# Performance work log

Hardware: AMD Instinct MI355X
Metric: run time of the kernel (lower is better)

The kernel has to match this reference:

```python
import jax, jax.numpy as jnp
import numpy as np

B, N, K = 2, 16384, 8
NH, HD, CH, KV_IN = 4, 32, 128, 128
EPS = 1e-5

def layer_norm(x, g, b):
    mu = x.mean(-1, keepdims=True)
    var = ((x - mu) ** 2).mean(-1, keepdims=True)
    return (x - mu) / jnp.sqrt(var + EPS) * g + b

def setup_inputs() -> dict:
    key = jax.random.key(0)
    ks = jax.random.split(key, 8)
    s = 0.02
    return {
        "query_in": jax.random.normal(ks[0], (B, N, CH), jnp.float32),
        "kv_in": jax.random.normal(ks[1], (B, N, K, KV_IN), jnp.float32),
        "w_kv": jax.random.normal(ks[2], (KV_IN, 2 * NH * HD), jnp.float32) * s,
        "w_q": jax.random.normal(ks[3], (CH, NH * HD), jnp.float32) * s,
        "w_mh": jax.random.normal(ks[4], (NH * HD, CH), jnp.float32) * s,
        "b_mh": jnp.zeros((CH,), jnp.float32),
        "w1": jax.random.normal(ks[5], (CH, CH), jnp.float32) * s,
        "b1": jnp.zeros((CH,), jnp.float32),
        "w2": jax.random.normal(ks[6], (CH, CH), jnp.float32) * s,
        "b2": jnp.zeros((CH,), jnp.float32),
        "ln1_g": jnp.ones((CH,), jnp.float32),
        "ln1_b": jnp.zeros((CH,), jnp.float32),
        "ln2_g": jnp.ones((CH,), jnp.float32),
        "ln2_b": jnp.zeros((CH,), jnp.float32),
    }

def reference(query_in, kv_in, w_kv, w_q, w_mh, b_mh, w1, b1, w2, b2,
              ln1_g, ln1_b, ln2_g, ln2_b):
    # q projection: [B,N,CH] -> [B,N,NH,HD]
    q = (query_in @ w_q).reshape(B, N, NH, HD)
    # kv projection: [B,N,K,KV_IN] -> [B,N,K,2,NH,HD]; chunk(2) on last dim
    kv = (kv_in @ w_kv).reshape(B, N, K, 2, NH, HD)
    k, v = kv[..., 0, :, :], kv[..., 1, :, :]  # each [B,N,K,NH,HD]
    # per-token local attention over its own K keys
    sim = jnp.einsum('bnhd,bnkhd->bnhk', q, k) / np.sqrt(HD).astype(np.float32)
    attn = jax.nn.softmax(sim, axis=-1)
    out = jnp.einsum('bnhk,bnkhd->bnhd', attn, v).reshape(B, N, NH * HD)
    out = out @ w_mh + b_mh
    res = layer_norm(out, ln1_g, ln1_b) + query_in
    # GELU MLP (torch nn.GELU default = exact erf form)
    mlp = jax.nn.gelu(res @ w1 + b1, approximate=False) @ w2 + b2
    return layer_norm(mlp + res, ln2_g, ln2_b)
```

## Files before the change

### kernel.cpp

```cpp
#include <hip/hip_runtime.h>
#include <hip/hip_fp16.h>

typedef _Float16 f16x8 __attribute__((ext_vector_type(8)));
typedef float f32x4 __attribute__((ext_vector_type(4)));
typedef unsigned int uint32;

#define LDW 136
#define TB  16

#define WAITLGKM() do { __builtin_amdgcn_s_waitcnt(0xC07F); __builtin_amdgcn_sched_barrier(0); } while(0)

#define BAR() do {                                          \
  asm volatile("s_waitcnt lgkmcnt(0)" ::: "memory");        \
  __builtin_amdgcn_sched_barrier(0);                        \
  __builtin_amdgcn_s_barrier();                             \
  __builtin_amdgcn_sched_barrier(0);                        \
} while (0)

union F16x8U { f16x8 v; __half2 h2[4]; uint2 u2[2]; uint4 u4; };

__device__ __forceinline__ uint32 pk2f(float a, float b) {
  __half2 h = __floats2half2_rn(a, b);
  return *reinterpret_cast<uint32*>(&h);
}
__device__ __forceinline__ float bcast(float v, int sl) {
  return __int_as_float(__builtin_amdgcn_readlane(__float_as_int(v), sl));
}
__device__ __forceinline__ float wred_sum(float v) {
  v += __shfl_xor(v, 32); v += __shfl_xor(v, 16); v += __shfl_xor(v, 8);
  v += __shfl_xor(v, 4);  v += __shfl_xor(v, 2);  v += __shfl_xor(v, 1);
  return v;
}
__device__ __forceinline__ f16x8 ldsv8(const __half* p) {
  return *reinterpret_cast<const f16x8*>(p);
}
__device__ __forceinline__ f32x4 mfma16(f16x8 a, f16x8 b, f32x4 c) {
  return __builtin_amdgcn_mfma_f32_16x16x32_f16(a, b, c, 0, 0, 0);
}
__device__ __forceinline__ void stp(__half* base, int fr, int fq, int nt, f32x4 a) {
  uint2 u; u.x = pk2f(a[0], a[1]); u.y = pk2f(a[2], a[3]);
  *reinterpret_cast<uint2*>(&base[fr * LDW + nt * 16 + fq * 4]) = u;
}

#define OFF_WQ   0
#define OFF_WK2  16384
#define OFF_WV   36864
#define OFF_WMH  53248
#define OFF_W1   69632
#define OFF_W2   86016
#define WS_HALVES 102400

__global__ void prep_weights(const float* __restrict__ wq, const float* __restrict__ wkv,
                             const float* __restrict__ wmh, const float* __restrict__ w1,
                             const float* __restrict__ w2, __half* __restrict__ ws) {
  int idx = blockIdx.x * 256 + threadIdx.x;
  if (idx >= WS_HALVES) return;
  float v;
  if (idx < OFF_WK2) {
    int t = idx, c = t >> 7, k = t & 127;
    v = wq[k * 128 + c];
  } else if (idx < OFF_WV) {
    int t = idx - OFF_WK2;
    int d = t % 40, row = t / 40;
    int h = row >> 7, i = row & 127;
    v = (d < 32) ? wkv[i * 256 + h * 32 + d] : 0.f;
  } else if (idx < OFF_WMH) {
    int t = idx - OFF_WV, c = t >> 7, k = t & 127;
    v = wkv[k * 256 + 128 + c];
  } else if (idx < OFF_W1) {
    int t = idx - OFF_WMH, c = t >> 7, k = t & 127;
    v = wmh[k * 128 + c];
  } else if (idx < OFF_W2) {
    int t = idx - OFF_W1, c = t >> 7, k = t & 127;
    v = w1[k * 128 + c];
  } else {
    int t = idx - OFF_W2, c = t >> 7, k = t & 127;
    v = w2[k * 128 + c];
  }
  ws[idx] = __float2half_rn(v);
}

#define LOADB2(GOFF, NT0, NT1, BF) do {                                          \
  _Pragma("unroll")                                                              \
  for (int t_ = 0; t_ < 2; ++t_) {                                               \
    int nt_ = t_ ? (NT1) : (NT0);                                                \
    _Pragma("unroll")                                                            \
    for (int ks_ = 0; ks_ < 4; ++ks_)                                            \
      BF[t_][ks_] = *reinterpret_cast<const f16x8*>(                             \
          wsv + (GOFF) + (nt_*16 + fr)*128 + ks_*32 + fq*8);                     \
  } } while (0)

#define GEMM2(AT, BF, ACC0, ACC1) do {                                           \
  _Pragma("unroll")                                                              \
  for (int ks_ = 0; ks_ < 4; ++ks_) {                                            \
    f16x8 b_ = ldsv8(&(AT)[fr * LDW + ks_ * 32 + fq * 8]);                       \
    ACC0 = mfma16(BF[0][ks_], b_, ACC0);                                         \
    ACC1 = mfma16(BF[1][ks_], b_, ACC1);                                         \
  } } while (0)

__global__ void __launch_bounds__(256, 6) ca_mfma(
    const float* __restrict__ xq, const float* __restrict__ kvin,
    const __half* __restrict__ wsv,
    const float* __restrict__ bmh, const float* __restrict__ b1,
    const float* __restrict__ b2,
    const float* __restrict__ g1, const float* __restrict__ bb1,
    const float* __restrict__ g2, const float* __restrict__ bb2,
    float* __restrict__ outp)
{
  __shared__ __half QWC[64 * LDW];
  __shared__ __half UBUF[2 * TB * LDW];

  const int tid = threadIdx.x;
  const int wv = tid >> 6, lane = tid & 63;
  const int fr = lane & 15, fq = lane >> 4;
  const int tb = blockIdx.x * TB;
  const int ltb = wv * 4;

  __half* Xh = UBUF;
  __half* Qb = UBUF + 2176;
  __half* Ob = UBUF;
  __half* Yb   = QWC;
  __half* RESb = QWC + 16 * LDW;
  __half* Hb   = QWC + 32 * LDW;
  __half* Vb   = QWC + 48 * LDW;

  const f32x4 ZZ = {0.f, 0.f, 0.f, 0.f};

  float4 pre[4];
  {
    const float4* kv4 = reinterpret_cast<const float4*>(kvin + (size_t)(tb + ltb) * 1024);
    pre[0] = kv4[2 * lane];       pre[1] = kv4[2 * lane + 1];
    pre[2] = kv4[2 * lane + 128]; pre[3] = kv4[2 * lane + 129];
  }
  f16x8 bf[2][4];
  LOADB2(OFF_WQ, wv, 4 + wv, bf);

  {
    int tok = tid >> 4, ko = (tid & 15) * 8;
    const float4* s0 = reinterpret_cast<const float4*>(xq + (size_t)(tb + tok) * 128 + ko);
    float4 a = s0[0], b = s0[1];
    uint4 u; u.x = pk2f(a.x, a.y); u.y = pk2f(a.z, a.w);
    u.z = pk2f(b.x, b.y); u.w = pk2f(b.z, b.w);
    *reinterpret_cast<uint4*>(&Xh[tok * LDW + ko]) = u;
  }
  BAR();

  {
    f32x4 aA = ZZ, aB = ZZ;
    GEMM2(Xh, bf, aA, aB);
    stp(Qb, fr, fq, wv, aA);
    stp(Qb, fr, fq, 4 + wv, aB);
  }
  f16x8 bq[8];
#pragma unroll
  for (int nt = 0; nt < 8; ++nt)
    bq[nt] = *reinterpret_cast<const f16x8*>(
        wsv + OFF_WK2 + (wv * 128 + nt * 16 + fr) * 40 + fq * 8);
  BAR();

  {
    f16x8 aq = ldsv8(&Qb[fr * LDW + wv * 32 + fq * 8]);
#pragma unroll
    for (int nt = 0; nt < 8; ++nt) {
      f32x4 acc = mfma16(bq[nt], aq, ZZ);
      uint2 u; u.x = pk2f(acc[0], acc[1]); u.y = pk2f(acc[2], acc[3]);
      *reinterpret_cast<uint2*>(&QWC[(wv * 16 + fr) * LDW + nt * 16 + fq * 4]) = u;
    }
  }
  BAR();

  {
    const int p = lane & 31, hh = p >> 3, kk = p & 7, hf = lane >> 5;
    const int kr = lane >> 4, i8 = (lane & 15) * 8;
    const int l2 = 2 * lane;
    __half* kvw = UBUF + wv * 1088;
#pragma unroll 1
    for (int lt = 0; lt < 4; ++lt) {
      const int ltok = ltb + lt;
      WAITLGKM();
      {
        uint4 u0, u1;
        u0.x = pk2f(pre[0].x, pre[0].y); u0.y = pk2f(pre[0].z, pre[0].w);
        u0.z = pk2f(pre[1].x, pre[1].y); u0.w = pk2f(pre[1].z, pre[1].w);
        u1.x = pk2f(pre[2].x, pre[2].y); u1.y = pk2f(pre[2].z, pre[2].w);
        u1.z = pk2f(pre[3].x, pre[3].y); u1.w = pk2f(pre[3].z, pre[3].w);
        *reinterpret_cast<uint4*>(&kvw[kr * LDW + i8]) = u0;
        *reinterpret_cast<uint4*>(&kvw[(4 + kr) * LDW + i8]) = u1;
      }
      if (lt < 3) {
        const float4* kv4 = reinterpret_cast<const float4*>(kvin + (size_t)(tb + ltok + 1) * 1024);
        pre[0] = kv4[2 * lane];       pre[1] = kv4[2 * lane + 1];
        pre[2] = kv4[2 * lane + 128]; pre[3] = kv4[2 * lane + 129];
      }
      WAITLGKM();
      const __half* qrow = &QWC[(hh * 16 + ltok) * LDW + hf * 64];
      const __half* krow = &kvw[kk * LDW + hf * 64];
      __half2 s0 = __floats2half2_rn(0.f, 0.f), s1 = s0;
#pragma unroll
      for (int e = 0; e < 8; ++e) {
        F16x8U q8, k8;
        q8.v = ldsv8(qrow + e * 8);
        k8.v = ldsv8(krow + e * 8);
        s0 = __hfma2(q8.h2[0], k8.h2[0], s0);
        s1 = __hfma2(q8.h2[1], k8.h2[1], s1);
        s0 = __hfma2(q8.h2[2], k8.h2[2], s0);
        s1 = __hfma2(q8.h2[3], k8.h2[3], s1);
      }
      s0 = __hadd2(s0, s1);
      float acc = (__low2float(s0) + __high2float(s0)) * 0.17677669529663687f;
      acc += __shfl_xor(acc, 32);
      float m = acc;
      m = fmaxf(m, __shfl_xor(m, 1));
      m = fmaxf(m, __shfl_xor(m, 2));
      m = fmaxf(m, __shfl_xor(m, 4));
      float e = __expf(acc - m);
      float sden = e;
      sden += __shfl_xor(sden, 1); sden += __shfl_xor(sden, 2); sden += __shfl_xor(sden, 4);
      float at = __fdividef(e, sden);
      __half2 kvc[8];
#pragma unroll
      for (int k = 0; k < 8; ++k)
        kvc[k] = *reinterpret_cast<const __half2*>(&kvw[k * LDW + l2]);
#pragma unroll
      for (int h = 0; h < 4; ++h) {
        float c0 = 0.f, c1 = 0.f;
#pragma unroll
        for (int k = 0; k < 8; ++k) {
          float a = bcast(at, h * 8 + k);
          float2 kf = __half22float2(kvc[k]);
          c0 = fmaf(a, kf.x, c0);
          c1 = fmaf(a, kf.y, c1);
        }
        *reinterpret_cast<__half2*>(&QWC[(h * 16 + ltok) * LDW + l2]) =
            __floats2half2_rn(c0, c1);
      }
    }
  }
  LOADB2(OFF_WV, wv, 4 + wv, bf);
  BAR();

  float2 xr[4];
#pragma unroll
  for (int lt = 0; lt < 4; ++lt) {
    int tok = tb + ltb + lt;
    xr[lt] = *reinterpret_cast<const float2*>(&xq[(size_t)tok * 128 + 2 * lane]);
  }
  {
    const int h1 = wv >> 1, h2 = 2 + (wv >> 1);
    f32x4 a1c = ZZ, a2c = ZZ;
#pragma unroll
    for (int ks = 0; ks < 4; ++ks) {
      f16x8 b1f = ldsv8(&QWC[(h1 * 16 + fr) * LDW + ks * 32 + fq * 8]);
      a1c = mfma16(bf[0][ks], b1f, a1c);
      f16x8 b2f = ldsv8(&QWC[(h2 * 16 + fr) * LDW + ks * 32 + fq * 8]);
      a2c = mfma16(bf[1][ks], b2f, a2c);
    }
    stp(Ob, fr, fq, wv, a1c);
    stp(Ob, fr, fq, 4 + wv, a2c);
  }
  LOADB2(OFF_WMH, wv, 4 + wv, bf);
  BAR();

  {
    f32x4 aA = ZZ, aB = ZZ;
    GEMM2(Ob, bf, aA, aB);
    stp(Yb, fr, fq, wv, aA);
    stp(Yb, fr, fq, 4 + wv, aB);
  }
  LOADB2(OFF_W1, wv, 4 + wv, bf);
  BAR();

  {
    const int l2 = 2 * lane;
    float2 bm = *reinterpret_cast<const float2*>(&bmh[l2]);
    float2 gg = *reinterpret_cast<const float2*>(&g1[l2]);
    float2 cc = *reinterpret_cast<const float2*>(&bb1[l2]);
#pragma unroll
    for (int lt = 0; lt < 4; ++lt) {
      int row = ltb + lt;
      float2 y = __half22float2(*reinterpret_cast<const __half2*>(&Yb[row * LDW + l2]));
      float v0 = y.x + bm.x, v1 = y.y + bm.y;
      float s = wred_sum(v0 + v1);
      float sq = wred_sum(v0 * v0 + v1 * v1);
      float mu = s * 0.0078125f;
      float var = sq * 0.0078125f - mu * mu;
      float rstd = rsqrtf(var + 1e-5f);
      float r0 = (v0 - mu) * rstd * gg.x + cc.x + xr[lt].x;
      float r1 = (v1 - mu) * rstd * gg.y + cc.y + xr[lt].y;
      *reinterpret_cast<__half2*>(&RESb[row * LDW + l2]) = __floats2half2_rn(r0, r1);
    }
  }
  BAR();

  {
    f32x4 aA = ZZ, aB = ZZ;
    GEMM2(RESb, bf, aA, aB);
    int c0 = wv * 16 + fq * 4, c1 = 64 + wv * 16 + fq * 4;
    float4 b1a = *reinterpret_cast<const float4*>(&b1[c0]);
    float4 b1b = *reinterpret_cast<const float4*>(&b1[c1]);
    uint2 ua, ub;
    float t0, t1;
    t0 = aA[0] + b1a.x; t0 = 0.5f * t0 * (1.f + erff(t0 * 0.70710678118654752f));
    t1 = aA[1] + b1a.y; t1 = 0.5f * t1 * (1.f + erff(t1 * 0.70710678118654752f));
    ua.x = pk2f(t0, t1);
    t0 = aA[2] + b1a.z; t0 = 0.5f * t0 * (1.f + erff(t0 * 0.70710678118654752f));
    t1 = aA[3] + b1a.w; t1 = 0.5f * t1 * (1.f + erff(t1 * 0.70710678118654752f));
    ua.y = pk2f(t0, t1);
    t0 = aB[0] + b1b.x; t0 = 0.5f * t0 * (1.f + erff(t0 * 0.70710678118654752f));
    t1 = aB[1] + b1b.y; t1 = 0.5f * t1 * (1.f + erff(t1 * 0.70710678118654752f));
    ub.x = pk2f(t0, t1);
    t0 = aB[2] + b1b.z; t0 = 0.5f * t0 * (1.f + erff(t0 * 0.70710678118654752f));
    t1 = aB[3] + b1b.w; t1 = 0.5f * t1 * (1.f + erff(t1 * 0.70710678118654752f));
    ub.y = pk2f(t0, t1);
    *reinterpret_cast<uint2*>(&Hb[fr * LDW + c0]) = ua;
    *reinterpret_cast<uint2*>(&Hb[fr * LDW + c1]) = ub;
  }
  LOADB2(OFF_W2, wv, 4 + wv, bf);
  BAR();

  {
    f32x4 aA = ZZ, aB = ZZ;
    GEMM2(Hb, bf, aA, aB);
    int c0 = wv * 16 + fq * 4, c1 = 64 + wv * 16 + fq * 4;
    float4 b2a = *reinterpret_cast<const float4*>(&b2[c0]);
    float4 b2b = *reinterpret_cast<const float4*>(&b2[c1]);
    F16x8U ra, rb;
    ra.u2[0] = *reinterpret_cast<const uint2*>(&RESb[fr * LDW + c0]);
    rb.u2[0] = *reinterpret_cast<const uint2*>(&RESb[fr * LDW + c1]);
    uint2 ua, ub;
    float2 p0 = __half22float2(ra.h2[0]), p1 = __half22float2(ra.h2[1]);
    ua.x = pk2f(aA[0] + b2a.x + p0.x, aA[1] + b2a.y + p0.y);
    ua.y = pk2f(aA[2] + b2a.z + p1.x, aA[3] + b2a.w + p1.y);
    float2 p2 = __half22float2(rb.h2[0]), p3 = __half22float2(rb.h2[1]);
    ub.x = pk2f(aB[0] + b2b.x + p2.x, aB[1] + b2b.y + p2.y);
    ub.y = pk2f(aB[2] + b2b.z + p3.x, aB[3] + b2b.w + p3.y);
    *reinterpret_cast<uint2*>(&Vb[fr * LDW + c0]) = ua;
    *reinterpret_cast<uint2*>(&Vb[fr * LDW + c1]) = ub;
  }
  BAR();

  {
    const int l2 = 2 * lane;
    float2 gg = *reinterpret_cast<const float2*>(&g2[l2]);
    float2 cc = *reinterpret_cast<const float2*>(&bb2[l2]);
#pragma unroll
    for (int lt = 0; lt < 4; ++lt) {
      int row = ltb + lt, tok = tb + row;
      float2 v = __half22float2(*reinterpret_cast<const __half2*>(&Vb[row * LDW + l2]));
      float s = wred_sum(v.x + v.y);
      float sq = wred_sum(v.x * v.x + v.y * v.y);
      float mu = s * 0.0078125f;
      float var = sq * 0.0078125f - mu * mu;
      float rstd = rsqrtf(var + 1e-5f);
      float2 o;
      o.x = (v.x - mu) * rstd * gg.x + cc.x;
      o.y = (v.y - mu) * rstd * gg.y + cc.y;
      *reinterpret_cast<float2*>(&outp[(size_t)tok * 128 + l2]) = o;
    }
  }
}

extern "C" void kernel_launch(void* const* d_in, const int* in_sizes, int n_in,
                              void* d_out, int out_size, void* d_ws, size_t ws_size,
                              hipStream_t stream) {
  const float* xq = (const float*)d_in[0];
  const float* kv = (const float*)d_in[1];
  const float* wkv = (const float*)d_in[2];
  const float* wq = (const float*)d_in[3];
  const float* wmh = (const float*)d_in[4];
  const float* bmh = (const float*)d_in[5];
  const float* w1 = (const float*)d_in[6];
  const float* b1 = (const float*)d_in[7];
  const float* w2 = (const float*)d_in[8];
  const float* b2 = (const float*)d_in[9];
  const float* g1 = (const float*)d_in[10];
  const float* bb1 = (const float*)d_in[11];
  const float* g2 = (const float*)d_in[12];
  const float* bb2 = (const float*)d_in[13];
  __half* ws = (__half*)d_ws;

  prep_weights<<<(WS_HALVES + 255) / 256, 256, 0, stream>>>(wq, wkv, wmh, w1, w2, ws);

  const int tokens = 32768;
  ca_mfma<<<tokens / TB, 256, 0, stream>>>(xq, kv, ws, bmh, b1, b2,
                                           g1, bb1, g2, bb2, (float*)d_out);
}
```

Before: 65.50 us.

## Compute per-token attention scores with MFMA and DPP-based softmax reductions

Replaces the per-lane half2 FMA dot products for the query-key scores with four 16x16x32 MFMA instructions. Rows are replicated heads and columns are replicated keys, so the full score tile sits in accumulator registers. The softmax max and sum reductions now use DPP row moves and ds_swizzle instead of shfl_xor. The attention weights are broadcast by readlane from the accumulator layout. wred_sum is also rewritten to use DPP row_shr, row_bcast and a final readlane, which trims LDS-based shuffle traffic in the layer norms. The score MFMA computes redundant rows and columns, and it depends on the swizzle and DPP patterns matching the MFMA output layout.

```diff
diff --git a/kernel.cpp b/kernel.cpp
--- a/kernel.cpp
+++ b/kernel.cpp
@@ -26,10 +26,23 @@
 __device__ __forceinline__ float bcast(float v, int sl) {
   return __int_as_float(__builtin_amdgcn_readlane(__float_as_int(v), sl));
 }
+template <int CTRL, int RMASK = 0xF, int BMASK = 0xF>
+__device__ __forceinline__ float dppmov(float v) {
+  return __int_as_float(__builtin_amdgcn_update_dpp(
+      0, __float_as_int(v), CTRL, RMASK, BMASK, true));
+}
+template <int PAT>
+__device__ __forceinline__ float swzf(float v) {
+  return __int_as_float(__builtin_amdgcn_ds_swizzle(__float_as_int(v), PAT));
+}
 __device__ __forceinline__ float wred_sum(float v) {
-  v += __shfl_xor(v, 32); v += __shfl_xor(v, 16); v += __shfl_xor(v, 8);
-  v += __shfl_xor(v, 4);  v += __shfl_xor(v, 2);  v += __shfl_xor(v, 1);
-  return v;
+  v += dppmov<0x111>(v);
+  v += dppmov<0x112>(v);
+  v += dppmov<0x114>(v);
+  v += dppmov<0x118>(v);
+  v += dppmov<0x142, 0xA>(v);
+  v += dppmov<0x143, 0xC>(v);
+  return __int_as_float(__builtin_amdgcn_readlane(__float_as_int(v), 63));
 }
 __device__ __forceinline__ f16x8 ldsv8(const __half* p) {
   return *reinterpret_cast<const f16x8*>(p);
@@ -170,9 +183,9 @@
   BAR();
 
   {
-    const int p = lane & 31, hh = p >> 3, kk = p & 7, hf = lane >> 5;
     const int kr = lane >> 4, i8 = (lane & 15) * 8;
     const int l2 = 2 * lane;
+    const float SCALE = 0.17677669529663687f;
     __half* kvw = UBUF + wv * 1088;
 #pragma unroll 1
     for (int lt = 0; lt < 4; ++lt) {
@@ -193,30 +206,26 @@
         pre[2] = kv4[2 * lane + 128]; pre[3] = kv4[2 * lane + 129];
       }
       WAITLGKM();
-      const __half* qrow = &QWC[(hh * 16 + ltok) * LDW + hf * 64];
-      const __half* krow = &kvw[kk * LDW + hf * 64];
-      __half2 s0 = __floats2half2_rn(0.f, 0.f), s1 = s0;
-#pragma unroll
-      for (int e = 0; e < 8; ++e) {
-        F16x8U q8, k8;
-        q8.v = ldsv8(qrow + e * 8);
-        k8.v = ldsv8(krow + e * 8);
-        s0 = __hfma2(q8.h2[0], k8.h2[0], s0);
-        s1 = __hfma2(q8.h2[1], k8.h2[1], s1);
-        s0 = __hfma2(q8.h2[2], k8.h2[2], s0);
-        s1 = __hfma2(q8.h2[3], k8.h2[3], s1);
-      }
-      s0 = __hadd2(s0, s1);
-      float acc = (__low2float(s0) + __high2float(s0)) * 0.17677669529663687f;
-      acc += __shfl_xor(acc, 32);
-      float m = acc;
-      m = fmaxf(m, __shfl_xor(m, 1));
-      m = fmaxf(m, __shfl_xor(m, 2));
-      m = fmaxf(m, __shfl_xor(m, 4));
-      float e = __expf(acc - m);
-      float sden = e;
-      sden += __shfl_xor(sden, 1); sden += __shfl_xor(sden, 2); sden += __shfl_xor(sden, 4);
-      float at = __fdividef(e, sden);
+      f32x4 acc = ZZ;
+#pragma unroll
+      for (int ks = 0; ks < 4; ++ks) {
+        f16x8 a_ = ldsv8(&QWC[((fr & 3) * 16 + ltok) * LDW + ks * 32 + fq * 8]);
+        f16x8 b_ = ldsv8(&kvw[(fr & 7) * LDW + ks * 32 + fq * 8]);
+        acc = mfma16(a_, b_, acc);
+      }
+      float at_[4];
+#pragma unroll
+      for (int r = 0; r < 4; ++r) {
+        float s = acc[r] * SCALE;
+        float mx = fmaxf(s, dppmov<0xB1>(s));
+        mx = fmaxf(mx, dppmov<0x4E>(mx));
+        mx = fmaxf(mx, swzf<0x101F>(mx));
+        float e = __expf(s - mx);
+        float dn = e + dppmov<0xB1>(e);
+        dn += dppmov<0x4E>(dn);
+        dn += swzf<0x101F>(dn);
+        at_[r] = __fdividef(e, dn);
+      }
       __half2 kvc[8];
 #pragma unroll
       for (int k = 0; k < 8; ++k)
@@ -226,7 +235,7 @@
         float c0 = 0.f, c1 = 0.f;
 #pragma unroll
         for (int k = 0; k < 8; ++k) {
-          float a = bcast(at, h * 8 + k);
+          float a = bcast(at_[h], k);
           float2 kf = __half22float2(kvc[k]);
           c0 = fmaf(a, kf.x, c0);
           c1 = fmaf(a, kf.y, c1);
```

Result: faster. 61.98 us (-5.4%).
